# Optimization experiments

Hardware: AMD Instinct MI355X
Metric: run time of the kernel (lower is better)

Reference implementation:

```python
import jax, jax.numpy as jnp
import numpy as np

P_FACTOR = 3.0
EPS = 1e-12  # torch F.normalize eps


def _l2norm(x):
    # torch.nn.functional.normalize(x, dim=1): x / max(||x||_2, eps)
    n = jnp.sqrt(jnp.sum(x * x, axis=1, keepdims=True))
    return x / jnp.maximum(n, EPS)


def setup_inputs() -> dict:
    key = jax.random.key(0)
    k1, k2, k3, k4, k5 = jax.random.split(key, 5)
    B, N, D_IN, D_RED, C = 8192, 16384, 1024, 512, 28
    return {
        "features": jax.random.normal(k1, (B, D_IN), dtype=jnp.float32),
        "ex_features": jax.random.normal(k2, (N, D_IN), dtype=jnp.float32),
        "g_w": jax.random.normal(k3, (D_RED, D_IN), dtype=jnp.float32) * 0.02,
        "g_b": jax.random.normal(k4, (D_RED,), dtype=jnp.float32) * 0.02,
        "ex_classes": jax.random.uniform(k5, (N, C), dtype=jnp.float32),
    }


def reference(features, ex_features, g_w, g_b, ex_classes):
    # g: Linear(input_dim -> dim_reduce)
    f = features @ g_w.T + g_b          # [B, D_red]
    ef = ex_features @ g_w.T + g_b      # [N, D_red]
    # cosine similarity
    s = _l2norm(f) @ _l2norm(ef).T      # [B, N]
    # power-sign activation: |s|^p * sign(s)
    a = jnp.power(jnp.abs(s), P_FACTOR) * jnp.sign(s)
    echo = a @ ex_classes               # [B, C]
    b = jnp.clip(jnp.sum(ex_classes, axis=0), 1.0, None)
    echo = jnp.clip(echo / b, 0.0, 1.0)
    return echo
```

## Files before the change

### kernel.cpp

```cpp
#include <hip/hip_runtime.h>
#include <stdint.h>

typedef __attribute__((ext_vector_type(4))) float f32x4;
typedef __attribute__((ext_vector_type(8))) short s16x8;

#define MFMA16(A, B, C) __builtin_amdgcn_mfma_f32_16x16x32_bf16(A, B, C, 0, 0, 0)
#define WAIT_VM(N) asm volatile("s_waitcnt vmcnt(" #N ")" ::: "memory")
#define WAIT_LGKM() asm volatile("s_waitcnt lgkmcnt(0)" ::: "memory")
#define BAR() __builtin_amdgcn_s_barrier()
#define SCHED_FENCE() __builtin_amdgcn_sched_barrier(0)
#define SP1() __builtin_amdgcn_s_setprio(1)
#define SP0() __builtin_amdgcn_s_setprio(0)

#define PHASE_SYNC(N) do { SCHED_FENCE(); WAIT_LGKM(); WAIT_VM(N); BAR(); SCHED_FENCE(); } while (0)
#define PHASE_SYNC_NOVM() do { SCHED_FENCE(); WAIT_LGKM(); BAR(); SCHED_FENCE(); } while (0)

__device__ __forceinline__ unsigned short f2bf(float x) {
  union { float f; unsigned u; } v; v.f = x;
  return (unsigned short)((v.u + 0x7fffu + ((v.u >> 16) & 1u)) >> 16);
}

__global__ void k_cast_bf16(const float* __restrict__ in, unsigned short* __restrict__ out, int n4) {
  int i = blockIdx.x * blockDim.x + threadIdx.x;
  const int stride = gridDim.x * blockDim.x;
  for (; i < n4; i += stride) {
    const float4 v = ((const float4*)in)[i];
    ushort4 o;
    o.x = f2bf(v.x); o.y = f2bf(v.y); o.z = f2bf(v.z); o.w = f2bf(v.w);
    ((ushort4*)out)[i] = o;
  }
}

__global__ void k_excT(const float* __restrict__ exc, unsigned short* __restrict__ excT,
                       float* __restrict__ bvec) {
  const int c = blockIdx.x;
  const int tid = threadIdx.x;
  float sum = 0.f;
  for (int j = tid; j < 16384; j += 256) {
    const float v = (c < 28) ? exc[(size_t)j * 28 + c] : 0.f;
    excT[(size_t)c * 16384 + j] = f2bf(v);
    sum += v;
  }
  #pragma unroll
  for (int o = 32; o; o >>= 1) sum += __shfl_down(sum, o, 64);
  __shared__ float wsum[4];
  if ((tid & 63) == 0) wsum[tid >> 6] = sum;
  __syncthreads();
  if (tid == 0 && c < 28) bvec[c] = fmaxf(wsum[0] + wsum[1] + wsum[2] + wsum[3], 1.0f);
}

__device__ __forceinline__ void stage_a(const unsigned short* __restrict__ src, int ld,
                                        unsigned short* smem, int dsoff, int w, int offsrc) {
  #pragma unroll
  for (int c = 0; c < 4; ++c)
    __builtin_amdgcn_global_load_lds(
        (const __attribute__((address_space(1))) unsigned int*)(src + offsrc + c * 64 * ld),
        (__attribute__((address_space(3))) unsigned int*)(smem + dsoff + c * 4096 + w * 512),
        16, 0, 0);
}
__device__ __forceinline__ void stage_b(const unsigned short* __restrict__ src, int ld,
                                        unsigned short* smem, int dsoff, int w, int offsrc) {
  #pragma unroll
  for (int c = 0; c < 2; ++c)
    __builtin_amdgcn_global_load_lds(
        (const __attribute__((address_space(1))) unsigned int*)(src + offsrc + c * 64 * ld),
        (__attribute__((address_space(3))) unsigned int*)(smem + dsoff + c * 4096 + w * 512),
        16, 0, 0);
}

__device__ __forceinline__ void mma_step_p(const unsigned short* smem, int ao, int bo,
                                           int wr, int wc, int r, int q, f32x4 acc[8][2]) {
  const int rx = r & 7;
  #pragma unroll
  for (int ks = 0; ks < 2; ++ks) {
    const int sb = ((ks * 4 + q) ^ rx) << 3;
    s16x8 bf[2];
    #pragma unroll
    for (int j = 0; j < 2; ++j)
      bf[j] = *(const s16x8*)(smem + bo + (wc * 32 + j * 16 + r) * 64 + sb);
    #pragma unroll
    for (int i = 0; i < 8; ++i) {
      const s16x8 af = *(const s16x8*)(smem + ao + (wr * 128 + i * 16 + r) * 64 + sb);
      #pragma unroll
      for (int j = 0; j < 2; ++j)
        acc[i][j] = MFMA16(af, bf[j], acc[i][j]);
    }
  }
}

#define PA0 0
#define PB0 16384
#define PA1 24576
#define PB1 40960

__global__ __launch_bounds__(512, 2) void k_proj(const unsigned short* __restrict__ featbf,
                                                 const unsigned short* __restrict__ exbf,
                                                 const unsigned short* __restrict__ gwbf,
                                                 const float* __restrict__ gb,
                                                 float* __restrict__ fall) {
  __shared__ __align__(16) unsigned short smem[49152];
  const int tid = threadIdx.x, w = tid >> 6, lane = tid & 63;
  const int wr = w >> 2, wc = w & 3, r = lane & 15, q = lane >> 4;
  const int offsrc = (w * 8 + (lane >> 3)) * 1024 + (((lane & 7) ^ (lane >> 3)) << 3);
  const int m0 = blockIdx.x * 256;
  const int n0 = blockIdx.y * 128;
  const unsigned short* Asrc = (m0 < 8192) ? (featbf + (size_t)m0 * 1024)
                                           : (exbf + (size_t)(m0 - 8192) * 1024);
  const unsigned short* Bsrc = gwbf + (size_t)n0 * 1024;
  f32x4 acc[8][2];
  #pragma unroll
  for (int i = 0; i < 8; ++i)
    #pragma unroll
    for (int j = 0; j < 2; ++j) acc[i][j] = {0.f, 0.f, 0.f, 0.f};

  stage_a(Asrc, 1024, smem, PA0, w, offsrc);
  stage_b(Bsrc, 1024, smem, PB0, w, offsrc);
  for (int t = 0; t < 15; ++t) {
    const int na = ((t + 1) & 1) ? PA1 : PA0, nbb = ((t + 1) & 1) ? PB1 : PB0;
    stage_a(Asrc + (t + 1) * 64, 1024, smem, na, w, offsrc);
    stage_b(Bsrc + (t + 1) * 64, 1024, smem, nbb, w, offsrc);
    WAIT_VM(6);
    BAR();
    mma_step_p(smem, (t & 1) ? PA1 : PA0, (t & 1) ? PB1 : PB0, wr, wc, r, q, acc);
    WAIT_LGKM();
    BAR();
  }
  WAIT_VM(0);
  BAR();
  mma_step_p(smem, PA1, PB1, wr, wc, r, q, acc);

  #pragma unroll
  for (int j = 0; j < 2; ++j) {
    const int col = n0 + wc * 32 + j * 16 + r;
    const float bias = gb[col];
    #pragma unroll
    for (int i = 0; i < 8; ++i) {
      const int row0 = m0 + wr * 128 + i * 16 + q * 4;
      #pragma unroll
      for (int t = 0; t < 4; ++t)
        fall[(size_t)(row0 + t) * 512 + col] = acc[i][j][t] + bias;
    }
  }
}

__global__ __launch_bounds__(256) void k_norm(const float* __restrict__ fall,
                                              unsigned short* __restrict__ fn) {
  const int row = blockIdx.x * 4 + (threadIdx.x >> 6);
  const int lane = threadIdx.x & 63;
  const float4* p = (const float4*)(fall + (size_t)row * 512) + lane * 2;
  const float4 v0 = p[0], v1 = p[1];
  float ss = v0.x * v0.x + v0.y * v0.y + v0.z * v0.z + v0.w * v0.w
           + v1.x * v1.x + v1.y * v1.y + v1.z * v1.z + v1.w * v1.w;
  #pragma unroll
  for (int o = 32; o; o >>= 1) ss += __shfl_xor(ss, o, 64);
  const float sc = 1.0f / fmaxf(sqrtf(ss), 1e-12f);
  ushort4 o0, o1;
  o0.x = f2bf(v0.x * sc); o0.y = f2bf(v0.y * sc); o0.z = f2bf(v0.z * sc); o0.w = f2bf(v0.w * sc);
  o1.x = f2bf(v1.x * sc); o1.y = f2bf(v1.y * sc); o1.z = f2bf(v1.z * sc); o1.w = f2bf(v1.w * sc);
  ushort4* qo = (ushort4*)(fn + (size_t)row * 512) + lane * 2;
  qo[0] = o0; qo[1] = o1;
}

#define BUFSZ 32768
#define EXL 65536

__device__ __forceinline__ void stage_half(const unsigned short* __restrict__ src,
                                           unsigned short* smem, int dsoff, int tid) {
  const int rowh = tid >> 3;
  const unsigned short* g = src + (size_t)rowh * 512 + (((tid & 7) ^ (rowh & 7)) << 3);
  __builtin_amdgcn_global_load_lds(
      (const __attribute__((address_space(1))) unsigned int*)g,
      (__attribute__((address_space(3))) unsigned int*)(smem + dsoff + tid * 8), 16, 0, 0);
  __builtin_amdgcn_global_load_lds(
      (const __attribute__((address_space(1))) unsigned int*)(g + 64 * 512),
      (__attribute__((address_space(3))) unsigned int*)(smem + dsoff + 4096 + tid * 8), 16, 0, 0);
}

__device__ __forceinline__ void stage_exc(const unsigned short* __restrict__ excTg, int c0,
                                          unsigned short* smem, int tid) {
  const int row = tid >> 5, b = tid & 31;
  const int sb = ((b & 24) | ((b ^ (row & 7)) & 7)) << 3;
  const unsigned short* g = excTg + (size_t)row * 16384 + c0 + sb;
  __builtin_amdgcn_global_load_lds(
      (const __attribute__((address_space(1))) unsigned int*)g,
      (__attribute__((address_space(3))) unsigned int*)(smem + EXL + tid * 8), 16, 0, 0);
  __builtin_amdgcn_global_load_lds(
      (const __attribute__((address_space(1))) unsigned int*)(g + 16 * 16384),
      (__attribute__((address_space(3))) unsigned int*)(smem + EXL + 4096 + tid * 8), 16, 0, 0);
}

__device__ __forceinline__ void ld_b_ks(const unsigned short* smem, int bufR, int ks,
                                        int wc, int r, int q, int rx, s16x8 b[2][2]) {
  const int sb = ((ks * 4 + q) ^ rx) << 3;
  #pragma unroll
  for (int nh = 0; nh < 2; ++nh)
    #pragma unroll
    for (int fj = 0; fj < 2; ++fj)
      b[nh][fj] = *(const s16x8*)(smem + bufR + 8192 + nh * 16384 + (wc * 32 + fj * 16 + r) * 64 + sb);
}
__device__ __forceinline__ void ld_a_q(const unsigned short* smem, int bufR, int MH, int ks,
                                       int wr, int r, int q, int rx, s16x8 a[4]) {
  const int sb = ((ks * 4 + q) ^ rx) << 3;
  #pragma unroll
  for (int fi = 0; fi < 4; ++fi)
    a[fi] = *(const s16x8*)(smem + bufR + MH * 16384 + (wr * 64 + fi * 16 + r) * 64 + sb);
}
__device__ __forceinline__ void mma16(const s16x8 a[4], const s16x8 b[2][2], f32x4 accm[2][4][2]) {
  #pragma unroll
  for (int fi = 0; fi < 4; ++fi)
    #pragma unroll
    for (int nh = 0; nh < 2; ++nh)
      #pragma unroll
      for (int fj = 0; fj < 2; ++fj)
        accm[nh][fi][fj] = MFMA16(a[fi], b[nh][fj], accm[nh][fi][fj]);
}

__global__ __launch_bounds__(512, 2) void k_fused(const unsigned short* __restrict__ fnall,
                                                  const unsigned short* __restrict__ excT,
                                                  float* __restrict__ partial) {
  __shared__ __align__(16) unsigned short smem[73728];
  const int tid = threadIdx.x, w = tid >> 6, lane = tid & 63;
  const int wr = w >> 2, wc = w & 3, r = lane & 15, q = lane >> 4, rx = r & 7;
  const int r0 = blockIdx.x * 256;
  const int nchunk = blockIdx.y;
  const unsigned short* Abase = fnall + (size_t)r0 * 512;
  const unsigned short* Ebase = fnall + (size_t)8192 * 512;
  unsigned short* aLb = smem + BUFSZ;

  f32x4 acc[2][2][4][2];
  f32x4 eacc[2][2];
  #pragma unroll
  for (int a = 0; a < 2; ++a)
    #pragma unroll
    for (int b = 0; b < 2; ++b) eacc[a][b] = {0.f, 0.f, 0.f, 0.f};

  {
    const unsigned short* B0p = Ebase + (size_t)(nchunk * 4) * 256 * 512;
    stage_half(Abase, smem, 0, tid);
    stage_half(B0p, smem, 8192, tid);
    stage_half(B0p + 128 * 512, smem, 24576, tid);
    stage_half(Abase + 128 * 512, smem, 16384, tid);
  }

  for (int jt = 0; jt < 4; ++jt) {
    #pragma unroll
    for (int a = 0; a < 2; ++a)
      #pragma unroll
      for (int b = 0; b < 2; ++b)
        #pragma unroll
        for (int fi = 0; fi < 4; ++fi)
          #pragma unroll
          for (int fj = 0; fj < 2; ++fj) acc[a][b][fi][fj] = {0.f, 0.f, 0.f, 0.f};

    for (int tk = 0; tk < 8; ++tk) {
      const int kt = jt * 8 + tk;
      const int bufR = (kt & 1) * BUFSZ, bufW = bufR ^ BUFSZ;
      const int kn = (kt + 1) & 31;
      const unsigned short* An = Abase + (kn & 7) * 64;
      const unsigned short* Bn = Ebase + (size_t)((nchunk * 4 + (kn >> 3)) * 256) * 512 + (kn & 7) * 64;
      s16x8 bk0[2][2], bk1[2][2], af[4];
      PHASE_SYNC(2);
      stage_half(An, smem, bufW + 0, tid);
      if (tk == 7) stage_exc(excT, (nchunk * 4 + jt) * 256, smem, tid);
      SP1();
      ld_b_ks(smem, bufR, 0, wc, r, q, rx, bk0);
      ld_a_q(smem, bufR, 0, 0, wr, r, q, rx, af);
      mma16(af, bk0, acc[0]);
      SP0();
      PHASE_SYNC(4);
      stage_half(Bn, smem, bufW + 8192, tid);
      SP1();
      ld_b_ks(smem, bufR, 1, wc, r, q, rx, bk1);
      ld_a_q(smem, bufR, 0, 1, wr, r, q, rx, af);
      mma16(af, bk1, acc[0]);
      SP0();
      PHASE_SYNC(4);
      stage_half(Bn + 128 * 512, smem, bufW + 24576, tid);
      SP1();
      ld_a_q(smem, bufR, 1, 0, wr, r, q, rx, af);
      mma16(af, bk0, acc[1]);
      SP0();
      PHASE_SYNC_NOVM();
      stage_half(An + 128 * 512, smem, bufW + 16384, tid);
      SP1();
      ld_a_q(smem, bufR, 1, 1, wr, r, q, rx, af);
      mma16(af, bk1, acc[1]);
      SP0();
    }

    SCHED_FENCE(); WAIT_LGKM(); WAIT_VM(6); BAR(); SCHED_FENCE();
    #pragma unroll
    for (int h = 0; h < 2; ++h) {
      #pragma unroll
      for (int nh = 0; nh < 2; ++nh)
        #pragma unroll
        for (int fi = 0; fi < 4; ++fi)
          #pragma unroll
          for (int fj = 0; fj < 2; ++fj) {
            const int colc = nh * 128 + wc * 32 + fj * 16 + r;
            const int cb = colc >> 3, cl = colc & 7;
            #pragma unroll
            for (int t2 = 0; t2 < 4; ++t2) {
              const int row = wr * 64 + fi * 16 + q * 4 + t2;
              const float v = acc[h][nh][fi][fj][t2];
              aLb[row * 256 + ((((cb & 24) | ((cb ^ (row & 7)) & 7)) << 3) | cl)] = f2bf(v * v * v);
            }
          }
      SCHED_FENCE(); WAIT_LGKM(); BAR(); SCHED_FENCE();
      {
        const int rE = w * 16 + r;
        const int re8 = rE & 7;
        #pragma unroll
        for (int kc = 0; kc < 8; ++kc) {
          const int kb = kc * 4 + q;
          const s16x8 af = *(const s16x8*)(aLb + rE * 256 + (((kb & 24) | ((kb ^ re8) & 7)) << 3));
          #pragma unroll
          for (int nj = 0; nj < 2; ++nj) {
            const s16x8 bfr = *(const s16x8*)(smem + EXL + (nj * 16 + r) * 256 +
                                              (((kb & 24) | ((kb ^ rx) & 7)) << 3));
            eacc[h][nj] = MFMA16(af, bfr, eacc[h][nj]);
          }
        }
      }
      SCHED_FENCE(); WAIT_LGKM(); BAR(); SCHED_FENCE();
    }
  }

  #pragma unroll
  for (int h = 0; h < 2; ++h)
    #pragma unroll
    for (int nj = 0; nj < 2; ++nj) {
      const int rb = r0 + h * 128 + w * 16 + q * 4;
      const int cls = nj * 16 + r;
      #pragma unroll
      for (int t = 0; t < 4; ++t)
        partial[((size_t)nchunk * 8192 + rb + t) * 32 + cls] = eacc[h][nj][t];
    }
}

__global__ void k_reduce(const float* __restrict__ partial, const float* __restrict__ bvec,
                         float* __restrict__ out) {
  const int idx = blockIdx.x * 256 + threadIdx.x;
  const int row = idx / 28, c = idx - row * 28;
  float s = 0.f;
  #pragma unroll
  for (int nc = 0; nc < 16; ++nc) s += partial[((size_t)nc * 8192 + row) * 32 + c];
  out[idx] = fminf(fmaxf(s / bvec[c], 0.f), 1.f);
}

extern "C" void kernel_launch(void* const* d_in, const int* in_sizes, int n_in,
                              void* d_out, int out_size, void* d_ws, size_t ws_size,
                              hipStream_t stream) {
  const float* features    = (const float*)d_in[0];
  const float* ex_features = (const float*)d_in[1];
  const float* g_w         = (const float*)d_in[2];
  const float* g_b         = (const float*)d_in[3];
  const float* ex_classes  = (const float*)d_in[4];
  float* out = (float*)d_out;
  char* ws = (char*)d_ws;

  unsigned short* featbf = (unsigned short*)(ws + 0);
  unsigned short* exbf   = (unsigned short*)(ws + 16777216);
  unsigned short* fnall  = (unsigned short*)(ws + 0);
  float* fall            = (float*)(ws + 50331648);
  float* partial         = (float*)(ws + 50331648);
  unsigned short* gwbf   = (unsigned short*)(ws + 100663296);
  unsigned short* excT   = (unsigned short*)(ws + 101711872);
  float* bvec            = (float*)(ws + 102760448);

  k_cast_bf16<<<2048, 256, 0, stream>>>(features, featbf, 8192 * 1024 / 4);
  k_cast_bf16<<<2048, 256, 0, stream>>>(ex_features, exbf, 16384 * 1024 / 4);
  k_cast_bf16<<<512, 256, 0, stream>>>(g_w, gwbf, 512 * 1024 / 4);
  k_excT<<<32, 256, 0, stream>>>(ex_classes, excT, bvec);
  k_proj<<<dim3(96, 4), 512, 0, stream>>>(featbf, exbf, gwbf, g_b, fall);
  k_norm<<<6144, 256, 0, stream>>>(fall, fnall);
  k_fused<<<dim3(32, 16), 512, 0, stream>>>(fnall, excT, partial);
  k_reduce<<<896, 256, 0, stream>>>(partial, bvec, out);
}
```

Before: 295.9 us.

## Restructure K-loop into two barrier phases with earlier bulk prefetch

Cuts the inner K-step from four barrier-separated phases to two. Three of the four next-tile half-loads are issued up front and each M-half's full MMA work runs per phase. The last K-step is peeled so the excT stage and the final prefetch (skipped on the last jt) are handled explicitly, with adjusted vmcnt waits. The aim is fewer workgroup barriers per tile. The cost is more outstanding loads and reloaded B fragments per phase, which adds LDS reads and register pressure.

```diff
diff --git a/kernel.cpp b/kernel.cpp
--- a/kernel.cpp
+++ b/kernel.cpp
@@ -13,7 +13,6 @@
 #define SP0() __builtin_amdgcn_s_setprio(0)
 
 #define PHASE_SYNC(N) do { SCHED_FENCE(); WAIT_LGKM(); WAIT_VM(N); BAR(); SCHED_FENCE(); } while (0)
-#define PHASE_SYNC_NOVM() do { SCHED_FENCE(); WAIT_LGKM(); BAR(); SCHED_FENCE(); } while (0)
 
 __device__ __forceinline__ unsigned short f2bf(float x) {
   union { float f; unsigned u; } v; v.f = x;
@@ -215,6 +214,18 @@
         accm[nh][fi][fj] = MFMA16(a[fi], b[nh][fj], accm[nh][fi][fj]);
 }
 
+__device__ __forceinline__ void mh_phase(const unsigned short* smem, int bufR, int MH,
+                                         int wr, int wc, int r, int q, int rx,
+                                         f32x4 accm[2][4][2]) {
+  s16x8 bf[2][2], af[4];
+  ld_b_ks(smem, bufR, 0, wc, r, q, rx, bf);
+  ld_a_q(smem, bufR, MH, 0, wr, r, q, rx, af);
+  mma16(af, bf, accm);
+  ld_b_ks(smem, bufR, 1, wc, r, q, rx, bf);
+  ld_a_q(smem, bufR, MH, 1, wr, r, q, rx, af);
+  mma16(af, bf, accm);
+}
+
 __global__ __launch_bounds__(512, 2) void k_fused(const unsigned short* __restrict__ fnall,
                                                   const unsigned short* __restrict__ excT,
                                                   float* __restrict__ partial) {
@@ -252,43 +263,43 @@
           #pragma unroll
           for (int fj = 0; fj < 2; ++fj) acc[a][b][fi][fj] = {0.f, 0.f, 0.f, 0.f};
 
-    for (int tk = 0; tk < 8; ++tk) {
+    for (int tk = 0; tk < 7; ++tk) {
       const int kt = jt * 8 + tk;
       const int bufR = (kt & 1) * BUFSZ, bufW = bufR ^ BUFSZ;
+      const int kn = kt + 1;
+      const unsigned short* An = Abase + (kn & 7) * 64;
+      const unsigned short* Bn = Ebase + (size_t)((nchunk * 4 + (kn >> 3)) * 256) * 512 + (kn & 7) * 64;
+      PHASE_SYNC(2);
+      stage_half(An, smem, bufW + 0, tid);
+      stage_half(Bn, smem, bufW + 8192, tid);
+      stage_half(Bn + 128 * 512, smem, bufW + 24576, tid);
+      SP1(); mh_phase(smem, bufR, 0, wr, wc, r, q, rx, acc[0]); SP0();
+      PHASE_SYNC(6);
+      stage_half(An + 128 * 512, smem, bufW + 16384, tid);
+      SP1(); mh_phase(smem, bufR, 1, wr, wc, r, q, rx, acc[1]); SP0();
+    }
+    {
+      const int kt = jt * 8 + 7;
+      const int bufR = BUFSZ, bufW = 0;
       const int kn = (kt + 1) & 31;
       const unsigned short* An = Abase + (kn & 7) * 64;
       const unsigned short* Bn = Ebase + (size_t)((nchunk * 4 + (kn >> 3)) * 256) * 512 + (kn & 7) * 64;
-      s16x8 bk0[2][2], bk1[2][2], af[4];
       PHASE_SYNC(2);
-      stage_half(An, smem, bufW + 0, tid);
-      if (tk == 7) stage_exc(excT, (nchunk * 4 + jt) * 256, smem, tid);
-      SP1();
-      ld_b_ks(smem, bufR, 0, wc, r, q, rx, bk0);
-      ld_a_q(smem, bufR, 0, 0, wr, r, q, rx, af);
-      mma16(af, bk0, acc[0]);
-      SP0();
-      PHASE_SYNC(4);
-      stage_half(Bn, smem, bufW + 8192, tid);
-      SP1();
-      ld_b_ks(smem, bufR, 1, wc, r, q, rx, bk1);
-      ld_a_q(smem, bufR, 0, 1, wr, r, q, rx, af);
-      mma16(af, bk1, acc[0]);
-      SP0();
-      PHASE_SYNC(4);
-      stage_half(Bn + 128 * 512, smem, bufW + 24576, tid);
-      SP1();
-      ld_a_q(smem, bufR, 1, 0, wr, r, q, rx, af);
-      mma16(af, bk0, acc[1]);
-      SP0();
-      PHASE_SYNC_NOVM();
-      stage_half(An + 128 * 512, smem, bufW + 16384, tid);
-      SP1();
-      ld_a_q(smem, bufR, 1, 1, wr, r, q, rx, af);
-      mma16(af, bk1, acc[1]);
-      SP0();
-    }
-
-    SCHED_FENCE(); WAIT_LGKM(); WAIT_VM(6); BAR(); SCHED_FENCE();
+      if (jt < 3) {
+        stage_half(An, smem, bufW + 0, tid);
+        stage_half(Bn, smem, bufW + 8192, tid);
+        stage_half(Bn + 128 * 512, smem, bufW + 24576, tid);
+      }
+      stage_exc(excT, (nchunk * 4 + jt) * 256, smem, tid);
+      SP1(); mh_phase(smem, bufR, 0, wr, wc, r, q, rx, acc[0]); SP0();
+      if (jt < 3) { PHASE_SYNC(8); } else { PHASE_SYNC(2); }
+      if (jt < 3) stage_half(An + 128 * 512, smem, bufW + 16384, tid);
+      SP1(); mh_phase(smem, bufR, 1, wr, wc, r, q, rx, acc[1]); SP0();
+    }
+
+    SCHED_FENCE(); WAIT_LGKM();
+    if (jt < 3) { WAIT_VM(2); } else { WAIT_VM(0); }
+    BAR(); SCHED_FENCE();
     #pragma unroll
     for (int h = 0; h < 2; ++h) {
       #pragma unroll
```

Measured after the change: 266.6 us. -9.9%, faster.
